# Optimization experiments

Measured on AMD Instinct MI355X. Metric: run time of the kernel, lower is better.

The kernel has to match this reference:

```python
import jax, jax.numpy as jnp
from jax import lax
import numpy as np

# dims (match init_kwargs config)
B, L, D = 32, 512, 32          # batch, seq_len, input_dim
H = 256                         # hidden_dim
E = 8                           # num_experts
PLEN, O = 96, 32                # pred_len, output_dim
LAT = 256                       # flow latent_dim
PD, NPROT = 64, 16              # prototype_dim, num_prototypes


def setup_inputs() -> dict:
    key = jax.random.key(0)
    ks = iter(jax.random.split(key, 40))
    def n(shape, scale=0.02):
        return (jax.random.normal(next(ks), shape, jnp.float32) * scale)
    inp = {
        'x': jax.random.normal(next(ks), (B, L, D), jnp.float32),
        # prototypes + projector (metric gating / diversity)
        'prototypes': n((NPROT, PD), 0.5),
        'Wp': n((PD, PD)), 'bp': jnp.zeros((PD,), jnp.float32),
        # expert_feature_extractor: Linear(7D->H), ReLU, Linear(H->PD), LayerNorm(PD)
        'Wf1': n((7 * D, H)), 'bf1': jnp.zeros((H,), jnp.float32),
        'Wf2': n((H, PD)), 'bf2': jnp.zeros((PD,), jnp.float32),
        'ln_g': jnp.ones((PD,), jnp.float32), 'ln_b': jnp.zeros((PD,), jnp.float32),
        # flow encoder (latent mapping of flattened window) + gating head
        'W1': n((L * D, H)), 'b1': jnp.zeros((H,), jnp.float32),
        'W2': n((H, LAT)), 'b2': jnp.zeros((LAT,), jnp.float32),
        'Wg': n((LAT, E)), 'bg': jnp.zeros((E,), jnp.float32),
        'log_temp': jnp.zeros((), jnp.float32),
        # stacked FFT+Mamba expert params (leading axis = expert)
        'Win': n((E, D, H)), 'b_in': jnp.zeros((E, H), jnp.float32),
        'Wfft': n((E, H, H)), 'b_fft': jnp.zeros((E, H), jnp.float32),
        'a_logit': n((E, H), 1.0),
        'Whead': n((E, H, PLEN * O)), 'b_head': jnp.zeros((E, PLEN * O), jnp.float32),
    }
    return inp


def _expert_features(x, Wf1, bf1, Wf2, bf2, ln_g, ln_b):
    # faithful to compute_expert_features: 7 per-channel stats -> MLP -> LayerNorm
    Lf = jnp.float32(x.shape[1])
    x_mean = x.mean(axis=1)
    x_std = x.std(axis=1, ddof=1)             # torch unbiased std
    x_min = x.min(axis=1)
    x_max = x.max(axis=1)
    x_diff_mean = jnp.diff(x, axis=1).mean(axis=1)
    x_trend = (x[:, -1, :] - x[:, 0, :]) / Lf
    x_fft_mag = jnp.abs(jnp.fft.fft(x, axis=1)).mean(axis=1)
    cf = jnp.concatenate([x_mean, x_std, x_min, x_max, x_diff_mean, x_trend, x_fft_mag], axis=1)
    h = jax.nn.relu(cf @ Wf1 + bf1)
    ef = h @ Wf2 + bf2
    mu = ef.mean(axis=-1, keepdims=True)
    var = ef.var(axis=-1, keepdims=True)
    return (ef - mu) / jnp.sqrt(var + 1e-5) * ln_g + ln_b


def reference(x, prototypes, Wp, bp, Wf1, bf1, Wf2, bf2, ln_g, ln_b,
              W1, b1, W2, b2, Wg, bg, log_temp,
              Win, b_in, Wfft, b_fft, a_logit, Whead, b_head):
    b, l, d = x.shape
    # --- metric-based gating ---
    ef = _expert_features(x, Wf1, bf1, Wf2, bf2, ln_g, ln_b)           # [B,PD]
    latent = jax.nn.relu(x.reshape(b, -1) @ W1 + b1) @ W2 + b2          # flow latent [B,LAT]
    lg = latent @ Wg + bg                                               # [B,E]
    proj = ef @ Wp + bp                                                 # prototype_projector
    d2 = ((proj[:, None, :] - prototypes[None, :, :]) ** 2).sum(-1)     # [B,NPROT]
    d2_per_expert = d2.reshape(b, E, NPROT // E).min(axis=-1)           # min dist to each expert's prototypes
    temp = jnp.clip(jnp.exp(log_temp), 0.1, 10.0)
    w = jax.nn.softmax((lg - d2_per_expert) / temp, axis=-1)            # [B,E]

    # --- FFT + Mamba-style experts (vmapped over stacked expert params) ---
    def expert(Win_e, b_in_e, Wfft_e, b_fft_e, a_logit_e, Whead_e, b_head_e):
        h = jnp.einsum('bld,dh->blh', x, Win_e) + b_in_e                # [B,L,H]
        f = jnp.einsum('blh,hk->blk', jnp.abs(jnp.fft.fft(h, axis=1)), Wfft_e) + b_fft_e
        u = jax.nn.relu(h + f)
        a = jax.nn.sigmoid(a_logit_e)                                   # per-channel decay
        def step(s, ut):
            s = a * s + (1.0 - a) * ut
            return s, None
        s_last, _ = lax.scan(step, jnp.zeros((b, H), x.dtype), jnp.swapaxes(u, 0, 1))
        return (s_last @ Whead_e + b_head_e).reshape(b, PLEN, O)

    outs = jax.vmap(expert)(Win, b_in, Wfft, b_fft, a_logit, Whead, b_head)  # [E,B,PLEN,O]
    y = jnp.einsum('be,ebpo->bpo', w, outs)
    return y
```

## Files before the change

### kernel.cpp

```cpp
#include <hip/hip_runtime.h>
#include <hip/hip_bf16.h>


typedef __hip_bfloat16 bf16;
typedef unsigned short u16;
typedef __attribute__((ext_vector_type(8))) short s8v;
typedef __attribute__((ext_vector_type(4))) float f4v;

#define MFMA_BF16(a,b,c) __builtin_amdgcn_mfma_f32_16x16x32_bf16(a,b,c,0,0,0)

#if __has_builtin(__builtin_amdgcn_sqrtf)
#define FSQRT(x) __builtin_amdgcn_sqrtf(x)
#else
#define FSQRT(x) sqrtf(x)
#endif
#if __has_builtin(__builtin_amdgcn_exp2f)
#define FEXP2(x) __builtin_amdgcn_exp2f(x)
#else
#define FEXP2(x) exp2f(x)
#endif
#if __has_builtin(__builtin_amdgcn_logf)
#define FLOG2(x) __builtin_amdgcn_logf(x)
#else
#define FLOG2(x) log2f(x)
#endif

#define GWF1 0
#define GW2  57344
#define GWF2 122880
#define GWP  139264
#define GPROT 143360
#define GWG  144384

__device__ __forceinline__ float bf2f(u16 u){
  union{ unsigned u32; float f; } w; w.u32 = ((unsigned)u) << 16; return w.f;
}
__device__ __forceinline__ u16 f2bf(float f){
  bf16 h = __float2bfloat16(f);
  union{ bf16 b; u16 u; } w; w.b = h; return w.u;
}
__device__ __forceinline__ u16 f2bf_fast(float f){
  union{ float f; unsigned u; } v; v.f = f;
  unsigned r = v.u + 0x7FFFu + ((v.u >> 16) & 1u);
  return (u16)(r >> 16);
}
__device__ __forceinline__ float ldg_(const void* p, long long i, bool bf){
  float r;
  if(bf) r = bf2f(((const u16*)p)[i]);
  else   r = ((const float*)p)[i];
  return r;
}
__device__ __forceinline__ bool bfflag(const void* ln_g){
  return ((const u16*)ln_g)[0] == 0x3F80;
}

__global__ __launch_bounds__(256) void ks1(const void* __restrict__ ln_g,
    const void* __restrict__ x,
    const void* __restrict__ Win, const void* __restrict__ Wfft,
    const void* __restrict__ W1, const void* __restrict__ Whead,
    const void* __restrict__ Wf1, const void* __restrict__ W2,
    const void* __restrict__ Wf2, const void* __restrict__ Wp,
    const void* __restrict__ prot, const void* __restrict__ Wg,
    u16* __restrict__ xbf,
    u16* __restrict__ WinTg, u16* __restrict__ WfftTg,
    u16* __restrict__ W1Tg, u16* __restrict__ WheadTg,
    u16* __restrict__ gw,
    u16* __restrict__ Xr, u16* __restrict__ Xi, float* __restrict__ cf){
  const bool bf = bfflag(ln_g);
  __shared__ float xs[512], re[512], im[512];
  __shared__ float twr[256], twi[256];
  __shared__ float r0s[4], r1s[4], r2s[4], r3s[4];
  __shared__ u16 tile[64][72];
  int BX = blockIdx.x, t = threadIdx.x;

  if(BX < 1024){
    int b = BX >> 5, d = BX & 31;
    {
      float rev = -(float)t * (1.f/512.f);
#if __has_builtin(__builtin_amdgcn_cosf) && __has_builtin(__builtin_amdgcn_sinf)
      twr[t] = __builtin_amdgcn_cosf(rev);
      twi[t] = __builtin_amdgcn_sinf(rev);
#else
      float ang = rev * 6.283185307179586f;
      twr[t] = cosf(ang); twi[t] = sinf(ang);
#endif
    }
    for(int i=t;i<512;i+=256){
      float v = ldg_(x, (long long)(b*512+i)*32 + d, bf);
      xs[i] = v;
      re[__brev((unsigned)i) >> 23] = v;
      im[i] = 0.f;
    }
    __syncthreads();
    float s=0.f, s2=0.f, mn=3.0e38f, mx=-3.0e38f;
    for(int i=t;i<512;i+=256){ float v=xs[i]; s+=v; s2+=v*v; mn=fminf(mn,v); mx=fmaxf(mx,v); }
    #pragma unroll
    for(int o=32;o>0;o>>=1){
      s  += __shfl_down(s,o);  s2 += __shfl_down(s2,o);
      mn = fminf(mn,__shfl_down(mn,o)); mx = fmaxf(mx,__shfl_down(mx,o));
    }
    int wv = t>>6, ln = t&63;
    if(ln==0){ r0s[wv]=s; r1s[wv]=s2; r2s[wv]=mn; r3s[wv]=mx; }
    __syncthreads();
    if(t==0){
      float S =r0s[0]+r0s[1]+r0s[2]+r0s[3];
      float S2=r1s[0]+r1s[1]+r1s[2]+r1s[3];
      float MN=fminf(fminf(r2s[0],r2s[1]),fminf(r2s[2],r2s[3]));
      float MX=fmaxf(fmaxf(r3s[0],r3s[1]),fmaxf(r3s[2],r3s[3]));
      float mean = S*(1.f/512.f);
      float var  = (S2 - S*S*(1.f/512.f))*(1.f/511.f);
      float* c = cf + b*224;
      c[d]      = mean;
      c[32+d]   = sqrtf(fmaxf(var,0.f));
      c[64+d]   = MN;
      c[96+d]   = MX;
      float dv = xs[511]-xs[0];
      c[128+d]  = dv*(1.f/511.f);
      c[160+d]  = dv*(1.f/512.f);
    }
    for(int st=1; st<=9; ++st){
      __syncthreads();
      int m = 1<<st, half = m>>1;
      int grp = t >> (st-1);
      int k   = t & (half-1);
      int i1 = grp*m + k, i2 = i1 + half;
      int ti_ = k << (9-st);
      float cs = twr[ti_], sn = twi[ti_];
      float ar=re[i1], ai=im[i1], br=re[i2], bi=im[i2];
      float tr = cs*br - sn*bi;
      float ti = cs*bi + sn*br;
      re[i1]=ar+tr; im[i1]=ai+ti;
      re[i2]=ar-tr; im[i2]=ai-ti;
    }
    __syncthreads();
    float ms=0.f;
    for(int i=t;i<512;i+=256){
      float rr=re[i], ii=im[i];
      long long o = (long long)(b*512+i)*32 + d;
      Xr[o]=f2bf(rr); Xi[o]=f2bf(ii);
      ms += FSQRT(rr*rr+ii*ii);
    }
    #pragma unroll
    for(int o=32;o>0;o>>=1) ms += __shfl_down(ms,o);
    if(ln==0) r0s[wv]=ms;
    __syncthreads();
    if(t==0) cf[b*224 + 192 + d] = (r0s[0]+r0s[1]+r0s[2]+r0s[3])*(1.f/512.f);
    return;
  }
  if(BX < 4111){
    int bx = BX - 1024;
    if(bx < 256){
      int i = bx*256 + t;
      int e = i >> 13, r = i & 8191;
      int c = r >> 5, d = r & 31;
      WinTg[i] = f2bf(ldg_(Win, (long long)e*8192 + d*256 + c, bf));
      return;
    }
    if(bx < 384){
      int idx = bx - 256;
      int e = idx >> 4, tl = idx & 15, kb = tl >> 2, cb = tl & 3;
      if(bf){
        for(int q=0;q<16;q++){
          int G = q*256 + t; int ki = G >> 6, ci = G & 63;
          tile[ci][ki] = ((const u16*)Wfft)[(long long)e*65536 + (long long)(kb*64+ki)*256 + cb*64+ci];
        }
      } else {
        for(int q=0;q<16;q++){
          int G = q*256 + t; int ki = G >> 6, ci = G & 63;
          tile[ci][ki] = f2bf(((const float*)Wfft)[(long long)e*65536 + (long long)(kb*64+ki)*256 + cb*64+ci]);
        }
      }
      __syncthreads();
      for(int q=0;q<16;q++){
        int G = q*256 + t; int ci = G >> 6, ki = G & 63;
        WfftTg[(long long)e*65536 + (long long)(cb*64+ci)*256 + kb*64+ki] = tile[ci][ki];
      }
      return;
    }
    if(bx < 1408){
      int idx = bx - 384;
      int kb = idx & 255, nb = idx >> 8;
      if(bf){
        for(int q=0;q<16;q++){
          int G = q*256 + t; int ki = G >> 6, ni = G & 63;
          tile[ni][ki] = ((const u16*)W1)[(long long)(kb*64+ki)*256 + nb*64+ni];
        }
      } else {
        for(int q=0;q<16;q++){
          int G = q*256 + t; int ki = G >> 6, ni = G & 63;
          tile[ni][ki] = f2bf(((const float*)W1)[(long long)(kb*64+ki)*256 + nb*64+ni]);
        }
      }
      __syncthreads();
      for(int q=0;q<16;q++){
        int G = q*256 + t; int ni = G >> 6, ki = G & 63;
        W1Tg[(long long)(nb*64+ni)*16384 + kb*64+ki] = tile[ni][ki];
      }
      return;
    }
    if(bx < 2944){
      int idx = bx - 1408;
      int e = idx / 192, rem = idx % 192;
      int kb = rem / 48, nb = rem % 48;
      if(bf){
        for(int q=0;q<16;q++){
          int G = q*256 + t; int ki = G >> 6, ni = G & 63;
          tile[ni][ki] = ((const u16*)Whead)[(long long)e*786432 + (long long)(kb*64+ki)*3072 + nb*64+ni];
        }
      } else {
        for(int q=0;q<16;q++){
          int G = q*256 + t; int ki = G >> 6, ni = G & 63;
          tile[ni][ki] = f2bf(((const float*)Whead)[(long long)e*786432 + (long long)(kb*64+ki)*3072 + nb*64+ni]);
        }
      }
      __syncthreads();
      for(int q=0;q<16;q++){
        int G = q*256 + t; int ni = G >> 6, ki = G & 63;
        WheadTg[(long long)e*786432 + (long long)(nb*64+ni)*256 + kb*64+ki] = tile[ni][ki];
      }
      return;
    }
    {
      int c = bx - 2944;
      const void* src; int dstbase, blkoff;
      if(c < 56)      { src=Wf1;  dstbase=GWF1;  blkoff=c; }
      else if(c <120) { src=W2;   dstbase=GW2;   blkoff=c-56; }
      else if(c <136) { src=Wf2;  dstbase=GWF2;  blkoff=c-120; }
      else if(c <140) { src=Wp;   dstbase=GWP;   blkoff=c-136; }
      else if(c <141) { src=prot; dstbase=GPROT; blkoff=0; }
      else            { src=Wg;   dstbase=GWG;   blkoff=c-141; }
      int i = blkoff*1024 + t*4;
      if(bf){
        ushort4 v = *(const ushort4*)((const u16*)src + i);
        *(ushort4*)(gw + dstbase + i) = v;
      } else {
        float4 f = *(const float4*)((const float*)src + i);
        ushort4 v; v.x=f2bf(f.x); v.y=f2bf(f.y); v.z=f2bf(f.z); v.w=f2bf(f.w);
        *(ushort4*)(gw + dstbase + i) = v;
      }
    }
    return;
  }
  {
    int i = ((BX-4111)*256 + t)*4;
    if(bf){
      ushort4 v = *(const ushort4*)((const u16*)x + i);
      *(ushort4*)(xbf+i) = v;
    } else {
      float4 f = *(const float4*)((const float*)x + i);
      ushort4 v; v.x=f2bf(f.x); v.y=f2bf(f.y); v.z=f2bf(f.z); v.w=f2bf(f.w);
      *(ushort4*)(xbf+i) = v;
    }
  }
}

__global__ __launch_bounds__(256) void ks2(const void* __restrict__ ln_g,
    const u16* __restrict__ xbf, const u16* __restrict__ Xr, const u16* __restrict__ Xi,
    const u16* __restrict__ WinTg, const u16* __restrict__ W1Tg,
    const void* __restrict__ b_in,
    float* __restrict__ psum, u16* __restrict__ hmagG){
  const bool bf = bfflag(ln_g);
  int BX = blockIdx.x, t = threadIdx.x;
  int w = t >> 6, lane = t & 63, quad = lane >> 4, l15 = lane & 15;
  const f4v zf = (f4v){0.f,0.f,0.f,0.f};
  __shared__ float binS[256];

  if(BX < 64){
    int kb = BX;
    f4v acc[2][4];
    #pragma unroll
    for(int mt=0;mt<2;mt++)
      #pragma unroll
      for(int nt=0;nt<4;nt++) acc[mt][nt] = zf;
    #pragma unroll
    for(int ks=0;ks<8;ks++){
      long long k = kb*256 + ks*32 + quad*8;
      s8v aF[2], bF[4];
      #pragma unroll
      for(int mt=0;mt<2;mt++)
        aF[mt] = *(const s8v*)(xbf + (long long)(mt*16 + l15)*16384 + k);
      #pragma unroll
      for(int nt=0;nt<4;nt++)
        bF[nt] = *(const s8v*)(W1Tg + (long long)(w*64 + nt*16 + l15)*16384 + k);
      #pragma unroll
      for(int mt=0;mt<2;mt++)
        #pragma unroll
        for(int nt=0;nt<4;nt++)
          acc[mt][nt] = MFMA_BF16(aF[mt], bF[nt], acc[mt][nt]);
    }
    float* po = psum + (long long)kb*8192;
    #pragma unroll
    for(int mt=0;mt<2;mt++)
      #pragma unroll
      for(int nt=0;nt<4;nt++)
        #pragma unroll
        for(int r=0;r<4;r++)
          po[(mt*16 + quad*4 + r)*256 + w*64 + nt*16 + l15] = acc[mt][nt][r];
    return;
  }
  {
    int bx = BX - 64;
    int e = bx >> 7, inner = bx & 127;
    int b = inner >> 2, half = (inner >> 1) & 1, kh = inner & 1;
    int row0 = b*512 + half*128;
    binS[t] = ldg_(b_in, e*256+t, bf);
    s8v xrF[2], xiF[2];
    #pragma unroll
    for(int nt=0;nt<2;nt++){
      long long row = row0 + w*32 + nt*16 + l15;
      xrF[nt] = *(const s8v*)(Xr + row*32 + quad*8);
      xiF[nt] = *(const s8v*)(Xi + row*32 + quad*8);
    }
    __syncthreads();
    u16* Ho = hmagG + (long long)((e<<6)|(b<<1)|half)*32768;
    #pragma unroll
    for(int kcl=0;kcl<2;kcl++){
      int k0 = (kh*2+kcl)*64;
      #pragma unroll
      for(int ct=0;ct<4;ct++){
        s8v wfr = *(const s8v*)(WinTg + ((long long)e*256 + k0 + ct*16 + l15)*32 + quad*8);
        #pragma unroll
        for(int nt=0;nt<2;nt++){
          f4v hr = MFMA_BF16(wfr, xrF[nt], zf);
          f4v hi = MFMA_BF16(wfr, xiF[nt], zf);
          int rowg = row0 + w*32 + nt*16 + l15;
          bool bin0 = ((rowg & 511) == 0);
          ushort4 pk;
          int cb4 = k0 + ct*16 + quad*4;
          float h0 = hr[0] + (bin0 ? 512.f*binS[cb4+0] : 0.f);
          float h1 = hr[1] + (bin0 ? 512.f*binS[cb4+1] : 0.f);
          float h2 = hr[2] + (bin0 ? 512.f*binS[cb4+2] : 0.f);
          float h3 = hr[3] + (bin0 ? 512.f*binS[cb4+3] : 0.f);
          pk.x = f2bf_fast(FSQRT(h0*h0 + hi[0]*hi[0]));
          pk.y = f2bf_fast(FSQRT(h1*h1 + hi[1]*hi[1]));
          pk.z = f2bf_fast(FSQRT(h2*h2 + hi[2]*hi[2]));
          pk.w = f2bf_fast(FSQRT(h3*h3 + hi[3]*hi[3]));
          *(ushort4*)&Ho[(w*32 + nt*16 + l15)*256 + cb4] = pk;
        }
      }
    }
  }
}

__global__ __launch_bounds__(256) void ks3(const void* __restrict__ ln_g,
    const float* __restrict__ cf, const float* __restrict__ psum,
    const u16* __restrict__ gw,
    const void* __restrict__ bf1, const void* __restrict__ b1,
    const u16* __restrict__ xbf, const u16* __restrict__ hmagG,
    const u16* __restrict__ WinTg, const u16* __restrict__ WfftTg,
    const void* __restrict__ b_in, const void* __restrict__ b_fft,
    const void* __restrict__ a_logit,
    float* __restrict__ hsf, float* __restrict__ h1f, float* __restrict__ sp){
  const bool bf = bfflag(ln_g);
  int BX = blockIdx.x, t = threadIdx.x;
  __shared__ __align__(16) u16 BsT[128][72];
  __shared__ float biasS[128], l2aS[128], aS[128];
  __shared__ float cfs[224];

  if(BX < 64){
    int bx = BX;
    if(bx < 32){
      int b = bx;
      float s0=0.f, s1=0.f, s2=0.f, s3=0.f;
      #pragma unroll
      for(int kb=0;kb<64;kb+=4){
        s0 += psum[(long long)(kb+0)*8192 + b*256 + t];
        s1 += psum[(long long)(kb+1)*8192 + b*256 + t];
        s2 += psum[(long long)(kb+2)*8192 + b*256 + t];
        s3 += psum[(long long)(kb+3)*8192 + b*256 + t];
      }
      hsf[b*256+t] = fmaxf((s0+s1)+(s2+s3) + ldg_(b1,t,bf), 0.f);
    } else {
      int b = bx - 32;
      if(t < 224) cfs[t] = cf[(long long)b*224 + t];
      __syncthreads();
      float a1 = ldg_(bf1, t, bf);
      const u16* Wp_ = gw + GWF1 + t;
      #pragma unroll 16
      for(int k=0;k<224;k++) a1 += cfs[k]*bf2f(Wp_[k*256]);
      h1f[b*256+t] = fmaxf(a1, 0.f);
    }
    return;
  }
  {
    int bx = BX - 64;
    int e = bx >> 7, inner = bx & 127;
    int b = inner >> 2, half = (inner >> 1) & 1, cb = inner & 1;
    int row0 = b*512 + half*128;
    int col0 = cb*128;
    int w = t >> 6, lane = t & 63, quad = lane >> 4, l15 = lane & 15;

    if(t < 128){
      int c = col0 + t;
      biasS[t] = ldg_(b_in, e*256+c, bf) + ldg_(b_fft, e*256+c, bf);
      float a = 1.f/(1.f+__expf(-ldg_(a_logit, e*256+c, bf)));
      a = fminf(fmaxf(a, 1e-12f), 0.99999988f);
      aS[t] = a;
      l2aS[t] = FLOG2(a);
    }
    const u16* Ab = hmagG + (long long)((e<<6)|(b<<1)|half)*32768;
    const f4v zf = (f4v){0.f,0.f,0.f,0.f};
    f4v acc[2][8];
    #pragma unroll
    for(int mt=0;mt<2;mt++)
      #pragma unroll
      for(int nt=0;nt<8;nt++) acc[mt][nt] = zf;

    for(int kc=0;kc<4;kc++){
      int k0 = kc*64;
      __syncthreads();
      #pragma unroll
      for(int q=0;q<4;q++){
        int G = q*256 + t;
        int c = G >> 3, k8 = (G & 7)*8;
        *(s8v*)&BsT[c][k8] = *(const s8v*)(WfftTg + ((long long)e*256 + col0 + c)*256 + k0 + k8);
      }
      __syncthreads();
      #pragma unroll
      for(int ks=0;ks<2;ks++){
        int kb = ks*32 + quad*8;
        s8v aF0 = *(const s8v*)(Ab + (w*32 + l15)*256 + k0 + kb);
        s8v aF1 = *(const s8v*)(Ab + (w*32 + 16 + l15)*256 + k0 + kb);
        #pragma unroll
        for(int nt=0;nt<8;nt++){
          s8v bF = *(const s8v*)&BsT[nt*16 + l15][kb];
          acc[0][nt] = MFMA_BF16(aF0, bF, acc[0][nt]);
          acc[1][nt] = MFMA_BF16(aF1, bF, acc[1][nt]);
        }
      }
    }
    s8v xF[2], xFm[2];
    #pragma unroll
    for(int mt=0;mt<2;mt++){
      long long rowO = (long long)row0 + w*32 + mt*16 + l15;
      xF[mt] = *(const s8v*)(xbf + rowO*32 + quad*8);
      int lin = half*128 + w*32 + mt*16 + l15;
      int lm  = (512 - lin) & 511;
      xFm[mt] = *(const s8v*)(xbf + ((long long)b*512 + lm)*32 + quad*8);
    }
    int l0base = half*128 + w*32 + quad*4;
    float mz = (l0base == 0) ? 0.f : 1.f;
    const f4v zf2 = (f4v){0.f,0.f,0.f,0.f};
    float part[8];
    #pragma unroll
    for(int nt=0;nt<8;nt++){
      s8v wfh = *(const s8v*)(WinTg + ((long long)e*256 + col0 + nt*16 + l15)*32 + quad*8);
      f4v hv0 = MFMA_BF16(xF[0],  wfh, zf2);
      f4v hv1 = MFMA_BF16(xF[1],  wfh, zf2);
      f4v hm0 = MFMA_BF16(xFm[0], wfh, zf2);
      f4v hm1 = MFMA_BF16(xFm[1], wfh, zf2);
      int cl = nt*16 + l15;
      float l2a = l2aS[cl], bias = biasS[cl], av = aS[cl];
      float inv_a = FEXP2(-l2a);
      float cO0 = FEXP2(l2a * (float)(511 - l0base));
      float cO1 = FEXP2(l2a * (float)(495 - l0base));
      float cM0 = FEXP2(l2a * (float)(l0base - 1));
      float cM1 = FEXP2(l2a * (float)(l0base + 15));
      float sum = 0.f;
      #pragma unroll
      for(int r=0;r<4;r++){
        float u0 = fmaxf(acc[0][nt][r] + hv0[r] + bias, 0.f);
        sum += u0 * cO0;
        float u1 = fmaxf(acc[1][nt][r] + hv1[r] + bias, 0.f);
        sum += u1 * cO1;
        float m0 = fmaxf(acc[0][nt][r] + hm0[r] + bias, 0.f);
        float w0 = m0 * cM0;
        if(r == 0) w0 *= mz;
        sum += w0;
        float m1 = fmaxf(acc[1][nt][r] + hm1[r] + bias, 0.f);
        sum += m1 * cM1;
        cO0 *= inv_a; cO1 *= inv_a; cM0 *= av; cM1 *= av;
      }
      part[nt] = sum;
    }
    __syncthreads();
    float (*redS)[132] = (float(*)[132])BsT;
    #pragma unroll
    for(int nt=0;nt<8;nt++)
      redS[w*4 + quad][nt*16 + l15] = part[nt];
    __syncthreads();
    if(t < 128){
      float tot = 0.f;
      #pragma unroll
      for(int i=0;i<16;i++) tot += redS[i][t];
      sp[e*16384 + (b*2 + half)*256 + col0 + t] = tot;
    }
  }
}

__global__ __launch_bounds__(256) void ks4(const void* __restrict__ ln_g,
    const float* __restrict__ hsf, const float* __restrict__ h1f,
    const u16* __restrict__ gw,
    const void* __restrict__ bf2, const void* __restrict__ ln_b,
    const void* __restrict__ bp, const void* __restrict__ b2,
    const void* __restrict__ bg, const void* __restrict__ log_temp,
    const float* __restrict__ sp, const void* __restrict__ a_logit,
    const void* __restrict__ b_in, const void* __restrict__ b_fft,
    const u16* __restrict__ xbf, const u16* __restrict__ Xr,
    const u16* __restrict__ Xi,
    const void* __restrict__ Win, const void* __restrict__ Wfft,
    float* __restrict__ wgt, u16* __restrict__ ssbf){
  const bool bf = bfflag(ln_g);
  int BX = blockIdx.x, t = threadIdx.x;
  __shared__ float hsL[256], h1L[256], latL[256], efL[64], prL[64];
  __shared__ float red[4][64];
  __shared__ float d2part[16][16], d2s[16], lgpart[32][8];
  __shared__ float hm[256];
  __shared__ float xr6[32], xi6[32], x6[32];

  if(BX < 32){
    int b = BX;
    hsL[t] = hsf[b*256+t];
    h1L[t] = h1f[b*256+t];
    __syncthreads();
    {
      float a = ldg_(b2, t, bf);
      const u16* W2p = gw + GW2 + t;
      #pragma unroll 16
      for(int k=0;k<256;k++) a += hsL[k]*bf2f(W2p[k*256]);
      latL[t] = a;
    }
    {
      int p = t>>6, j = t&63;
      float acc = 0.f;
      const u16* Wf2p = gw + GWF2 + p*64*64 + j;
      #pragma unroll 16
      for(int i=0;i<64;i++) acc += h1L[p*64+i]*bf2f(Wf2p[i*64]);
      red[p][j] = acc;
    }
    __syncthreads();
    if(t < 64){
      float a2 = red[0][t]+red[1][t]+red[2][t]+red[3][t] + ldg_(bf2,t,bf);
      float sm=a2, sq=a2*a2;
      #pragma unroll
      for(int o=32;o>0;o>>=1){ sm += __shfl_xor(sm,o); sq += __shfl_xor(sq,o); }
      float mu  = sm*(1.f/64.f);
      float var = sq*(1.f/64.f) - mu*mu;
      efL[t] = (a2-mu)*rsqrtf(fmaxf(var,0.f)+1e-5f)*ldg_(ln_g,t,bf) + ldg_(ln_b,t,bf);
      float p_acc = ldg_(bp, t, bf);
      const u16* Wpp = gw + GWP + t;
      #pragma unroll 16
      for(int k=0;k<64;k++) p_acc += efL[k]*bf2f(Wpp[k*64]);
      prL[t] = p_acc;
    }
    {
      int part = t>>3, e = t&7;
      float gp = 0.f;
      const u16* Wgp = gw + GWG + e;
      #pragma unroll
      for(int i=0;i<8;i++){
        int k = part*8 + i;
        gp += latL[k]*bf2f(Wgp[k*8]);
      }
      lgpart[part][e] = gp;
    }
    __syncthreads();
    {
      int p = t>>4, q4 = t&15;
      float dd = 0.f;
      #pragma unroll
      for(int i=0;i<4;i++){
        int d = q4*4 + i;
        float df = prL[d] - bf2f(gw[GPROT + p*64 + d]);
        dd += df*df;
      }
      d2part[p][q4] = dd;
    }
    __syncthreads();
    if(t < 16){
      float s = 0.f;
      #pragma unroll
      for(int i=0;i<16;i++) s += d2part[t][i];
      d2s[t] = s;
    }
    __syncthreads();
    if(t < 8){
      float g = ldg_(bg, t, bf);
      #pragma unroll
      for(int p=0;p<32;p++) g += lgpart[p][t];
      float d2pe = fminf(d2s[2*t], d2s[2*t+1]);
      float temp = fminf(fmaxf(__expf(ldg_(log_temp,0,bf)), 0.1f), 10.f);
      float v = (g - d2pe) / temp;
      float m = v;
      m = fmaxf(m, __shfl_xor(m,1));
      m = fmaxf(m, __shfl_xor(m,2));
      m = fmaxf(m, __shfl_xor(m,4));
      float ex = __expf(v-m);
      float sum = ex;
      sum += __shfl_xor(sum,1);
      sum += __shfl_xor(sum,2);
      sum += __shfl_xor(sum,4);
      wgt[b*8+t] = ex/sum;
    }
    return;
  }
  {
    int bx = BX - 32;
    int e = bx >> 5, b = bx & 31, j = t;
    if(j < 32){
      long long o = ((long long)(b*512 + 256))*32 + j;
      xr6[j] = bf2f(Xr[o]);
      xi6[j] = bf2f(Xi[o]);
      x6[j]  = bf2f(xbf[o]);
    }
    __syncthreads();
    float sr=0.f, si=0.f, hx=0.f;
    if(bf){
      const u16* Wn = (const u16*)Win + (long long)e*8192 + j;
      #pragma unroll 8
      for(int d=0; d<32; d++){
        float wv = bf2f(Wn[d*256]);
        sr += xr6[d]*wv; si += xi6[d]*wv; hx += x6[d]*wv;
      }
    } else {
      const float* Wn = (const float*)Win + (long long)e*8192 + j;
      #pragma unroll 8
      for(int d=0; d<32; d++){
        float wv = Wn[d*256];
        sr += xr6[d]*wv; si += xi6[d]*wv; hx += x6[d]*wv;
      }
    }
    hm[j] = FSQRT(sr*sr + si*si);
    __syncthreads();
    float f = 0.f;
    if(bf){
      const u16* Wf = (const u16*)Wfft + (long long)e*65536 + j;
      #pragma unroll 8
      for(int k=0;k<256;k++) f += hm[k]*bf2f(Wf[(long long)k*256]);
    } else {
      const float* Wf = (const float*)Wfft + (long long)e*65536 + j;
      #pragma unroll 8
      for(int k=0;k<256;k++) f += hm[k]*Wf[(long long)k*256];
    }
    float a = 1.f/(1.f+__expf(-ldg_(a_logit, e*256+j, bf)));
    a = fminf(fmaxf(a, 1e-12f), 0.99999988f);
    float l2a = FLOG2(a);
    float u = fmaxf(hx + f + ldg_(b_in,e*256+j,bf) + ldg_(b_fft,e*256+j,bf), 0.f);
    float contrib = u * FEXP2(l2a * 255.f);
    const float* spe = sp + e*16384 + b*2*256;
    float sum = spe[j] + spe[256+j] + contrib;
    ssbf[(e*32+b)*256 + j] = f2bf((1.f-a)*sum);
  }
}

__global__ __launch_bounds__(256) void k6_mfma(
    const u16* __restrict__ ssbf, const u16* __restrict__ WheadTg,
    float* __restrict__ yaccE){
  int nb = blockIdx.x, e = blockIdx.y;
  int t = threadIdx.x;
  int w = t >> 6, lane = t & 63, quad = lane >> 4, l15 = lane & 15;
  const f4v zf = (f4v){0.f,0.f,0.f,0.f};
  f4v acc[2][2];
  #pragma unroll
  for(int mt=0;mt<2;mt++)
    #pragma unroll
    for(int nt=0;nt<2;nt++) acc[mt][nt] = zf;
  #pragma unroll
  for(int ks=0;ks<8;ks++){
    int k = ks*32 + quad*8;
    s8v aF[2], bF[2];
    #pragma unroll
    for(int mt=0;mt<2;mt++)
      aF[mt] = *(const s8v*)(ssbf + (long long)(e*32 + mt*16 + l15)*256 + k);
    #pragma unroll
    for(int nt=0;nt<2;nt++)
      bF[nt] = *(const s8v*)(WheadTg + ((long long)e*3072 + nb*128 + w*32 + nt*16 + l15)*256 + k);
    #pragma unroll
    for(int mt=0;mt<2;mt++)
      #pragma unroll
      for(int nt=0;nt<2;nt++)
        acc[mt][nt] = MFMA_BF16(aF[mt], bF[nt], acc[mt][nt]);
  }
  float* yo = yaccE + (long long)e*98304;
  #pragma unroll
  for(int mt=0;mt<2;mt++)
    #pragma unroll
    for(int nt=0;nt<2;nt++){
      int col = nb*128 + w*32 + nt*16 + l15;
      #pragma unroll
      for(int r=0;r<4;r++){
        int b = mt*16 + quad*4 + r;
        yo[b*3072 + col] = acc[mt][nt][r];
      }
    }
}

__global__ void k7_out(const void* __restrict__ ln_g,
                       const float* __restrict__ yaccE,
                       const float* __restrict__ wgt,
                       const void* __restrict__ b_head,
                       void* __restrict__ out){
  const bool bf = bfflag(ln_g);
  int i = blockIdx.x*256 + threadIdx.x;
  int b = i / 3072, col = i - b*3072;
  float v = 0.f;
  #pragma unroll
  for(int e=0;e<8;e++)
    v += wgt[b*8+e]*(yaccE[(long long)e*98304 + i] + ldg_(b_head, (long long)e*3072+col, bf));
  if(bf) ((u16*)out)[i] = f2bf(v);
  else   ((float*)out)[i] = v;
}

extern "C" void kernel_launch(void* const* d_in, const int* in_sizes, int n_in,
                              void* d_out, int out_size, void* d_ws, size_t ws_size,
                              hipStream_t stream){
  const void* x       = d_in[0];
  const void* prot    = d_in[1];
  const void* Wp      = d_in[2];
  const void* bp      = d_in[3];
  const void* Wf1     = d_in[4];
  const void* bf1     = d_in[5];
  const void* Wf2     = d_in[6];
  const void* bf2     = d_in[7];
  const void* ln_g    = d_in[8];
  const void* ln_b    = d_in[9];
  const void* W1      = d_in[10];
  const void* b1      = d_in[11];
  const void* W2      = d_in[12];
  const void* b2      = d_in[13];
  const void* Wg      = d_in[14];
  const void* bg      = d_in[15];
  const void* log_temp= d_in[16];
  const void* Win     = d_in[17];
  const void* b_in    = d_in[18];
  const void* Wfft    = d_in[19];
  const void* b_fft   = d_in[20];
  const void* a_logit = d_in[21];
  const void* Whead   = d_in[22];
  const void* b_head  = d_in[23];

  float* ws      = (float*)d_ws;
  float* cf      = ws;
  float* wgt     = cf + 7168;
  float* sp      = wgt + 256;
  float* hsf     = sp + 131072;
  float* h1f     = hsf + 8192;
  float* yaccE   = sp + 262144;
  float* psum    = yaccE + 786432;
  u16*   Xr      = (u16*)(psum + 524288);
  u16*   Xi      = Xr + 524288;
  u16*   xbf     = Xi + 524288;
  u16*   WinTg   = xbf + 524288;
  u16*   WfftTg  = WinTg + 65536;
  u16*   W1Tg    = WfftTg + 524288;
  u16*   WheadTg = W1Tg + 4194304;
  u16*   ssbf    = WheadTg + 6291456;
  u16*   gw      = ssbf + 65536;
  u16*   hmagG   = gw + 146432;

  ks1 <<<dim3(4623), dim3(256), 0, stream>>>(ln_g, x, Win, Wfft, W1, Whead,
                                             Wf1, W2, Wf2, Wp, prot, Wg,
                                             xbf, WinTg, WfftTg, W1Tg, WheadTg, gw,
                                             Xr, Xi, cf);
  ks2 <<<dim3(1088), dim3(256), 0, stream>>>(ln_g, xbf, Xr, Xi, WinTg, W1Tg,
                                             b_in, psum, hmagG);
  ks3 <<<dim3(1088), dim3(256), 0, stream>>>(ln_g, cf, psum, gw, bf1, b1,
                                             xbf, hmagG, WinTg, WfftTg,
                                             b_in, b_fft, a_logit,
                                             hsf, h1f, sp);
  ks4 <<<dim3(288),  dim3(256), 0, stream>>>(ln_g, hsf, h1f, gw, bf2, ln_b,
                                             bp, b2, bg, log_temp,
                                             sp, a_logit, b_in, b_fft,
                                             xbf, Xr, Xi, Win, Wfft,
                                             wgt, ssbf);
  k6_mfma <<<dim3(24,8), dim3(256), 0, stream>>>(ssbf, WheadTg, yaccE);
  k7_out  <<<dim3(384),  dim3(256), 0, stream>>>(ln_g, yaccE, wgt, b_head, d_out);
}
```

Before: 204.9 us.

## Fold gating and expert tail into earlier kernels; fuse head GEMM with mixture

Moves the h1 feature MLP and the per-expert last-step contribution into ks2, and the gating softmax into ks3. The head GEMM and the weighted expert mixture become one kernel, k67, which loops over experts, builds the scaled state in shared memory and writes the output directly. This drops two launches and the yaccE, hsf and ssbf intermediates. In exchange, the fused head kernel runs only 24 blocks that walk all 8 experts in sequence, so far fewer CUs share the Whead streaming.

```diff
diff --git a/kernel.cpp b/kernel.cpp
--- a/kernel.cpp
+++ b/kernel.cpp
@@ -257,13 +257,20 @@
 __global__ __launch_bounds__(256) void ks2(const void* __restrict__ ln_g,
     const u16* __restrict__ xbf, const u16* __restrict__ Xr, const u16* __restrict__ Xi,
     const u16* __restrict__ WinTg, const u16* __restrict__ W1Tg,
-    const void* __restrict__ b_in,
-    float* __restrict__ psum, u16* __restrict__ hmagG){
+    const u16* __restrict__ gw, const float* __restrict__ cf,
+    const void* __restrict__ bf1, const void* __restrict__ b_in,
+    const void* __restrict__ b_fft, const void* __restrict__ a_logit,
+    const void* __restrict__ Win, const void* __restrict__ Wfft,
+    float* __restrict__ psum, u16* __restrict__ hmagG,
+    float* __restrict__ h1f, float* __restrict__ contrib){
   const bool bf = bfflag(ln_g);
   int BX = blockIdx.x, t = threadIdx.x;
   int w = t >> 6, lane = t & 63, quad = lane >> 4, l15 = lane & 15;
   const f4v zf = (f4v){0.f,0.f,0.f,0.f};
   __shared__ float binS[256];
+  __shared__ float cfs[224];
+  __shared__ float hm[256];
+  __shared__ float xr6[32], xi6[32], x6[32];
 
   if(BX < 64){
     int kb = BX;
@@ -298,7 +305,7 @@
           po[(mt*16 + quad*4 + r)*256 + w*64 + nt*16 + l15] = acc[mt][nt][r];
     return;
   }
-  {
+  if(BX < 1088){
     int bx = BX - 64;
     int e = bx >> 7, inner = bx & 127;
     int b = inner >> 2, half = (inner >> 1) & 1, kh = inner & 1;
@@ -339,28 +346,88 @@
         }
       }
     }
+    return;
+  }
+  if(BX < 1120){
+    int b = BX - 1088;
+    if(t < 224) cfs[t] = cf[(long long)b*224 + t];
+    __syncthreads();
+    float a1 = ldg_(bf1, t, bf);
+    const u16* Wp_ = gw + GWF1 + t;
+    #pragma unroll 16
+    for(int k=0;k<224;k++) a1 += cfs[k]*bf2f(Wp_[k*256]);
+    h1f[b*256+t] = fmaxf(a1, 0.f);
+    return;
+  }
+  {
+    int bx = BX - 1120;
+    int e = bx >> 5, b = bx & 31, j = t;
+    if(j < 32){
+      long long o = ((long long)(b*512 + 256))*32 + j;
+      xr6[j] = bf2f(Xr[o]);
+      xi6[j] = bf2f(Xi[o]);
+      x6[j]  = bf2f(xbf[o]);
+    }
+    __syncthreads();
+    float sr=0.f, si=0.f, hx=0.f;
+    if(bf){
+      const u16* Wn = (const u16*)Win + (long long)e*8192 + j;
+      #pragma unroll 8
+      for(int d=0; d<32; d++){
+        float wv = bf2f(Wn[d*256]);
+        sr += xr6[d]*wv; si += xi6[d]*wv; hx += x6[d]*wv;
+      }
+    } else {
+      const float* Wn = (const float*)Win + (long long)e*8192 + j;
+      #pragma unroll 8
+      for(int d=0; d<32; d++){
+        float wv = Wn[d*256];
+        sr += xr6[d]*wv; si += xi6[d]*wv; hx += x6[d]*wv;
+      }
+    }
+    hm[j] = FSQRT(sr*sr + si*si);
+    __syncthreads();
+    float f = 0.f;
+    if(bf){
+      const u16* Wf = (const u16*)Wfft + (long long)e*65536 + j;
+      #pragma unroll 8
+      for(int k=0;k<256;k++) f += hm[k]*bf2f(Wf[(long long)k*256]);
+    } else {
+      const float* Wf = (const float*)Wfft + (long long)e*65536 + j;
+      #pragma unroll 8
+      for(int k=0;k<256;k++) f += hm[k]*Wf[(long long)k*256];
+    }
+    float a = 1.f/(1.f+__expf(-ldg_(a_logit, e*256+j, bf)));
+    a = fminf(fmaxf(a, 1e-12f), 0.99999988f);
+    float l2a = FLOG2(a);
+    float u = fmaxf(hx + f + ldg_(b_in,e*256+j,bf) + ldg_(b_fft,e*256+j,bf), 0.f);
+    contrib[(e*32+b)*256 + j] = u * FEXP2(l2a * 255.f);
   }
 }
 
 __global__ __launch_bounds__(256) void ks3(const void* __restrict__ ln_g,
-    const float* __restrict__ cf, const float* __restrict__ psum,
+    const float* __restrict__ psum, const float* __restrict__ h1f,
     const u16* __restrict__ gw,
-    const void* __restrict__ bf1, const void* __restrict__ b1,
+    const void* __restrict__ b1, const void* __restrict__ bf2,
+    const void* __restrict__ ln_b, const void* __restrict__ bp,
+    const void* __restrict__ b2, const void* __restrict__ bg,
+    const void* __restrict__ log_temp,
     const u16* __restrict__ xbf, const u16* __restrict__ hmagG,
     const u16* __restrict__ WinTg, const u16* __restrict__ WfftTg,
     const void* __restrict__ b_in, const void* __restrict__ b_fft,
     const void* __restrict__ a_logit,
-    float* __restrict__ hsf, float* __restrict__ h1f, float* __restrict__ sp){
+    float* __restrict__ wgt, float* __restrict__ sp){
   const bool bf = bfflag(ln_g);
   int BX = blockIdx.x, t = threadIdx.x;
   __shared__ __align__(16) u16 BsT[128][72];
   __shared__ float biasS[128], l2aS[128], aS[128];
-  __shared__ float cfs[224];
-
-  if(BX < 64){
-    int bx = BX;
-    if(bx < 32){
-      int b = bx;
+  __shared__ float hsL[256], h1L[256], latL[256], efL[64], prL[64];
+  __shared__ float red[4][64];
+  __shared__ float d2part[16][16], d2s[16], lgpart[32][8];
+
+  if(BX < 32){
+    int b = BX;
+    {
       float s0=0.f, s1=0.f, s2=0.f, s3=0.f;
       #pragma unroll
       for(int kb=0;kb<64;kb+=4){
@@ -369,21 +436,93 @@
         s2 += psum[(long long)(kb+2)*8192 + b*256 + t];
         s3 += psum[(long long)(kb+3)*8192 + b*256 + t];
       }
-      hsf[b*256+t] = fmaxf((s0+s1)+(s2+s3) + ldg_(b1,t,bf), 0.f);
-    } else {
-      int b = bx - 32;
-      if(t < 224) cfs[t] = cf[(long long)b*224 + t];
-      __syncthreads();
-      float a1 = ldg_(bf1, t, bf);
-      const u16* Wp_ = gw + GWF1 + t;
+      hsL[t] = fmaxf((s0+s1)+(s2+s3) + ldg_(b1,t,bf), 0.f);
+    }
+    h1L[t] = h1f[b*256+t];
+    __syncthreads();
+    {
+      float a = ldg_(b2, t, bf);
+      const u16* W2p = gw + GW2 + t;
       #pragma unroll 16
-      for(int k=0;k<224;k++) a1 += cfs[k]*bf2f(Wp_[k*256]);
-      h1f[b*256+t] = fmaxf(a1, 0.f);
+      for(int k=0;k<256;k++) a += hsL[k]*bf2f(W2p[k*256]);
+      latL[t] = a;
+    }
+    {
+      int p = t>>6, j = t&63;
+      float acc = 0.f;
+      const u16* Wf2p = gw + GWF2 + p*64*64 + j;
+      #pragma unroll 16
+      for(int i=0;i<64;i++) acc += h1L[p*64+i]*bf2f(Wf2p[i*64]);
+      red[p][j] = acc;
+    }
+    __syncthreads();
+    if(t < 64){
+      float a2 = red[0][t]+red[1][t]+red[2][t]+red[3][t] + ldg_(bf2,t,bf);
+      float sm=a2, sq=a2*a2;
+      #pragma unroll
+      for(int o=32;o>0;o>>=1){ sm += __shfl_xor(sm,o); sq += __shfl_xor(sq,o); }
+      float mu  = sm*(1.f/64.f);
+      float var = sq*(1.f/64.f) - mu*mu;
+      efL[t] = (a2-mu)*rsqrtf(fmaxf(var,0.f)+1e-5f)*ldg_(ln_g,t,bf) + ldg_(ln_b,t,bf);
+      float p_acc = ldg_(bp, t, bf);
+      const u16* Wpp = gw + GWP + t;
+      #pragma unroll 16
+      for(int k=0;k<64;k++) p_acc += efL[k]*bf2f(Wpp[k*64]);
+      prL[t] = p_acc;
+    }
+    {
+      int part = t>>3, e = t&7;
+      float gp = 0.f;
+      const u16* Wgp = gw + GWG + e;
+      #pragma unroll
+      for(int i=0;i<8;i++){
+        int k = part*8 + i;
+        gp += latL[k]*bf2f(Wgp[k*8]);
+      }
+      lgpart[part][e] = gp;
+    }
+    __syncthreads();
+    {
+      int p = t>>4, q4 = t&15;
+      float dd = 0.f;
+      #pragma unroll
+      for(int i=0;i<4;i++){
+        int d = q4*4 + i;
+        float df = prL[d] - bf2f(gw[GPROT + p*64 + d]);
+        dd += df*df;
+      }
+      d2part[p][q4] = dd;
+    }
+    __syncthreads();
+    if(t < 16){
+      float s = 0.f;
+      #pragma unroll
+      for(int i=0;i<16;i++) s += d2part[t][i];
+      d2s[t] = s;
+    }
+    __syncthreads();
+    if(t < 8){
+      float g = ldg_(bg, t, bf);
+      #pragma unroll
+      for(int p=0;p<32;p++) g += lgpart[p][t];
+      float d2pe = fminf(d2s[2*t], d2s[2*t+1]);
+      float temp = fminf(fmaxf(__expf(ldg_(log_temp,0,bf)), 0.1f), 10.f);
+      float v = (g - d2pe) / temp;
+      float m = v;
+      m = fmaxf(m, __shfl_xor(m,1));
+      m = fmaxf(m, __shfl_xor(m,2));
+      m = fmaxf(m, __shfl_xor(m,4));
+      float ex = __expf(v-m);
+      float sum = ex;
+      sum += __shfl_xor(sum,1);
+      sum += __shfl_xor(sum,2);
+      sum += __shfl_xor(sum,4);
+      wgt[b*8+t] = ex/sum;
     }
     return;
   }
   {
-    int bx = BX - 64;
+    int bx = BX - 32;
     int e = bx >> 7, inner = bx & 127;
     int b = inner >> 2, half = (inner >> 1) & 1, cb = inner & 1;
     int row0 = b*512 + half*128;
@@ -488,190 +627,78 @@
   }
 }
 
-__global__ __launch_bounds__(256) void ks4(const void* __restrict__ ln_g,
-    const float* __restrict__ hsf, const float* __restrict__ h1f,
-    const u16* __restrict__ gw,
-    const void* __restrict__ bf2, const void* __restrict__ ln_b,
-    const void* __restrict__ bp, const void* __restrict__ b2,
-    const void* __restrict__ bg, const void* __restrict__ log_temp,
-    const float* __restrict__ sp, const void* __restrict__ a_logit,
-    const void* __restrict__ b_in, const void* __restrict__ b_fft,
-    const u16* __restrict__ xbf, const u16* __restrict__ Xr,
-    const u16* __restrict__ Xi,
-    const void* __restrict__ Win, const void* __restrict__ Wfft,
-    float* __restrict__ wgt, u16* __restrict__ ssbf){
+__global__ __launch_bounds__(256) void k67(const void* __restrict__ ln_g,
+    const float* __restrict__ sp, const float* __restrict__ contrib,
+    const float* __restrict__ wgt, const void* __restrict__ a_logit,
+    const u16* __restrict__ WheadTg, const void* __restrict__ b_head,
+    void* __restrict__ out){
   const bool bf = bfflag(ln_g);
-  int BX = blockIdx.x, t = threadIdx.x;
-  __shared__ float hsL[256], h1L[256], latL[256], efL[64], prL[64];
-  __shared__ float red[4][64];
-  __shared__ float d2part[16][16], d2s[16], lgpart[32][8];
-  __shared__ float hm[256];
-  __shared__ float xr6[32], xi6[32], x6[32];
-
-  if(BX < 32){
-    int b = BX;
-    hsL[t] = hsf[b*256+t];
-    h1L[t] = h1f[b*256+t];
-    __syncthreads();
-    {
-      float a = ldg_(b2, t, bf);
-      const u16* W2p = gw + GW2 + t;
-      #pragma unroll 16
-      for(int k=0;k<256;k++) a += hsL[k]*bf2f(W2p[k*256]);
-      latL[t] = a;
-    }
-    {
-      int p = t>>6, j = t&63;
-      float acc = 0.f;
-      const u16* Wf2p = gw + GWF2 + p*64*64 + j;
-      #pragma unroll 16
-      for(int i=0;i<64;i++) acc += h1L[p*64+i]*bf2f(Wf2p[i*64]);
-      red[p][j] = acc;
-    }
-    __syncthreads();
-    if(t < 64){
-      float a2 = red[0][t]+red[1][t]+red[2][t]+red[3][t] + ldg_(bf2,t,bf);
-      float sm=a2, sq=a2*a2;
-      #pragma unroll
-      for(int o=32;o>0;o>>=1){ sm += __shfl_xor(sm,o); sq += __shfl_xor(sq,o); }
-      float mu  = sm*(1.f/64.f);
-      float var = sq*(1.f/64.f) - mu*mu;
-      efL[t] = (a2-mu)*rsqrtf(fmaxf(var,0.f)+1e-5f)*ldg_(ln_g,t,bf) + ldg_(ln_b,t,bf);
-      float p_acc = ldg_(bp, t, bf);
-      const u16* Wpp = gw + GWP + t;
-      #pragma unroll 16
-      for(int k=0;k<64;k++) p_acc += efL[k]*bf2f(Wpp[k*64]);
-      prL[t] = p_acc;
-    }
-    {
-      int part = t>>3, e = t&7;
-      float gp = 0.f;
-      const u16* Wgp = gw + GWG + e;
-      #pragma unroll
-      for(int i=0;i<8;i++){
-        int k = part*8 + i;
-        gp += latL[k]*bf2f(Wgp[k*8]);
-      }
-      lgpart[part][e] = gp;
-    }
-    __syncthreads();
-    {
-      int p = t>>4, q4 = t&15;
-      float dd = 0.f;
-      #pragma unroll
-      for(int i=0;i<4;i++){
-        int d = q4*4 + i;
-        float df = prL[d] - bf2f(gw[GPROT + p*64 + d]);
-        dd += df*df;
-      }
-      d2part[p][q4] = dd;
-    }
-    __syncthreads();
-    if(t < 16){
-      float s = 0.f;
-      #pragma unroll
-      for(int i=0;i<16;i++) s += d2part[t][i];
-      d2s[t] = s;
-    }
-    __syncthreads();
-    if(t < 8){
-      float g = ldg_(bg, t, bf);
-      #pragma unroll
-      for(int p=0;p<32;p++) g += lgpart[p][t];
-      float d2pe = fminf(d2s[2*t], d2s[2*t+1]);
-      float temp = fminf(fmaxf(__expf(ldg_(log_temp,0,bf)), 0.1f), 10.f);
-      float v = (g - d2pe) / temp;
-      float m = v;
-      m = fmaxf(m, __shfl_xor(m,1));
-      m = fmaxf(m, __shfl_xor(m,2));
-      m = fmaxf(m, __shfl_xor(m,4));
-      float ex = __expf(v-m);
-      float sum = ex;
-      sum += __shfl_xor(sum,1);
-      sum += __shfl_xor(sum,2);
-      sum += __shfl_xor(sum,4);
-      wgt[b*8+t] = ex/sum;
-    }
-    return;
-  }
-  {
-    int bx = BX - 32;
-    int e = bx >> 5, b = bx & 31, j = t;
-    if(j < 32){
-      long long o = ((long long)(b*512 + 256))*32 + j;
-      xr6[j] = bf2f(Xr[o]);
-      xi6[j] = bf2f(Xi[o]);
-      x6[j]  = bf2f(xbf[o]);
-    }
-    __syncthreads();
-    float sr=0.f, si=0.f, hx=0.f;
-    if(bf){
-      const u16* Wn = (const u16*)Win + (long long)e*8192 + j;
-      #pragma unroll 8
-      for(int d=0; d<32; d++){
-        float wv = bf2f(Wn[d*256]);
-        sr += xr6[d]*wv; si += xi6[d]*wv; hx += x6[d]*wv;
-      }
-    } else {
-      const float* Wn = (const float*)Win + (long long)e*8192 + j;
-      #pragma unroll 8
-      for(int d=0; d<32; d++){
-        float wv = Wn[d*256];
-        sr += xr6[d]*wv; si += xi6[d]*wv; hx += x6[d]*wv;
-      }
-    }
-    hm[j] = FSQRT(sr*sr + si*si);
-    __syncthreads();
-    float f = 0.f;
-    if(bf){
-      const u16* Wf = (const u16*)Wfft + (long long)e*65536 + j;
-      #pragma unroll 8
-      for(int k=0;k<256;k++) f += hm[k]*bf2f(Wf[(long long)k*256]);
-    } else {
-      const float* Wf = (const float*)Wfft + (long long)e*65536 + j;
-      #pragma unroll 8
-      for(int k=0;k<256;k++) f += hm[k]*Wf[(long long)k*256];
-    }
-    float a = 1.f/(1.f+__expf(-ldg_(a_logit, e*256+j, bf)));
+  int nb = blockIdx.x, t = threadIdx.x;
+  int w = t >> 6, lane = t & 63, quad = lane >> 4, l15 = lane & 15;
+  __shared__ __align__(16) u16 ssS[32][264];
+  __shared__ float omaS[2048];
+  __shared__ float wgtS[256];
+
+  wgtS[t] = wgt[t];
+  #pragma unroll
+  for(int q=0;q<8;q++){
+    int idx = q*256 + t;
+    float a = 1.f/(1.f+__expf(-ldg_(a_logit, idx, bf)));
     a = fminf(fmaxf(a, 1e-12f), 0.99999988f);
-    float l2a = FLOG2(a);
-    float u = fmaxf(hx + f + ldg_(b_in,e*256+j,bf) + ldg_(b_fft,e*256+j,bf), 0.f);
-    float contrib = u * FEXP2(l2a * 255.f);
-    const float* spe = sp + e*16384 + b*2*256;
-    float sum = spe[j] + spe[256+j] + contrib;
-    ssbf[(e*32+b)*256 + j] = f2bf((1.f-a)*sum);
-  }
-}
-
-__global__ __launch_bounds__(256) void k6_mfma(
-    const u16* __restrict__ ssbf, const u16* __restrict__ WheadTg,
-    float* __restrict__ yaccE){
-  int nb = blockIdx.x, e = blockIdx.y;
-  int t = threadIdx.x;
-  int w = t >> 6, lane = t & 63, quad = lane >> 4, l15 = lane & 15;
+    omaS[idx] = 1.f - a;
+  }
   const f4v zf = (f4v){0.f,0.f,0.f,0.f};
   f4v acc[2][2];
   #pragma unroll
   for(int mt=0;mt<2;mt++)
     #pragma unroll
     for(int nt=0;nt<2;nt++) acc[mt][nt] = zf;
-  #pragma unroll
-  for(int ks=0;ks<8;ks++){
-    int k = ks*32 + quad*8;
-    s8v aF[2], bF[2];
+
+  for(int e=0;e<8;e++){
+    __syncthreads();
+    {
+      float oma = omaS[e*256 + t];
+      const float* sp0 = sp + e*16384 + t;
+      const float* cb  = contrib + e*8192 + t;
+      #pragma unroll
+      for(int q=0;q<32;q++){
+        float v = oma*(sp0[q*512] + sp0[q*512+256] + cb[q*256]);
+        ssS[q][t] = f2bf(v);
+      }
+    }
+    __syncthreads();
+    f4v tmp[2][2];
     #pragma unroll
     for(int mt=0;mt<2;mt++)
-      aF[mt] = *(const s8v*)(ssbf + (long long)(e*32 + mt*16 + l15)*256 + k);
-    #pragma unroll
-    for(int nt=0;nt<2;nt++)
-      bF[nt] = *(const s8v*)(WheadTg + ((long long)e*3072 + nb*128 + w*32 + nt*16 + l15)*256 + k);
-    #pragma unroll
-    for(int mt=0;mt<2;mt++)
+      #pragma unroll
+      for(int nt=0;nt<2;nt++) tmp[mt][nt] = zf;
+    #pragma unroll
+    for(int ks=0;ks<8;ks++){
+      int k = ks*32 + quad*8;
+      s8v aF0 = *(const s8v*)&ssS[l15][k];
+      s8v aF1 = *(const s8v*)&ssS[16 + l15][k];
+      s8v bF[2];
       #pragma unroll
       for(int nt=0;nt<2;nt++)
-        acc[mt][nt] = MFMA_BF16(aF[mt], bF[nt], acc[mt][nt]);
-  }
-  float* yo = yaccE + (long long)e*98304;
+        bF[nt] = *(const s8v*)(WheadTg + ((long long)e*3072 + nb*128 + w*32 + nt*16 + l15)*256 + k);
+      tmp[0][0] = MFMA_BF16(aF0, bF[0], tmp[0][0]);
+      tmp[0][1] = MFMA_BF16(aF0, bF[1], tmp[0][1]);
+      tmp[1][0] = MFMA_BF16(aF1, bF[0], tmp[1][0]);
+      tmp[1][1] = MFMA_BF16(aF1, bF[1], tmp[1][1]);
+    }
+    #pragma unroll
+    for(int nt=0;nt<2;nt++){
+      int col = nb*128 + w*32 + nt*16 + l15;
+      float bh = ldg_(b_head, (long long)e*3072 + col, bf);
+      #pragma unroll
+      for(int mt=0;mt<2;mt++)
+        #pragma unroll
+        for(int r=0;r<4;r++){
+          int b = mt*16 + quad*4 + r;
+          acc[mt][nt][r] += wgtS[b*8+e]*(tmp[mt][nt][r] + bh);
+        }
+    }
+  }
   #pragma unroll
   for(int mt=0;mt<2;mt++)
     #pragma unroll
@@ -680,25 +707,11 @@
       #pragma unroll
       for(int r=0;r<4;r++){
         int b = mt*16 + quad*4 + r;
-        yo[b*3072 + col] = acc[mt][nt][r];
-      }
-    }
-}
-
-__global__ void k7_out(const void* __restrict__ ln_g,
-                       const float* __restrict__ yaccE,
-                       const float* __restrict__ wgt,
-                       const void* __restrict__ b_head,
-                       void* __restrict__ out){
-  const bool bf = bfflag(ln_g);
-  int i = blockIdx.x*256 + threadIdx.x;
-  int b = i / 3072, col = i - b*3072;
-  float v = 0.f;
-  #pragma unroll
-  for(int e=0;e<8;e++)
-    v += wgt[b*8+e]*(yaccE[(long long)e*98304 + i] + ldg_(b_head, (long long)e*3072+col, bf));
-  if(bf) ((u16*)out)[i] = f2bf(v);
-  else   ((float*)out)[i] = v;
+        long long i = (long long)b*3072 + col;
+        if(bf) ((u16*)out)[i] = f2bf(acc[mt][nt][r]);
+        else   ((float*)out)[i] = acc[mt][nt][r];
+      }
+    }
 }
 
 extern "C" void kernel_launch(void* const* d_in, const int* in_sizes, int n_in,
@@ -733,10 +746,9 @@
   float* cf      = ws;
   float* wgt     = cf + 7168;
   float* sp      = wgt + 256;
-  float* hsf     = sp + 131072;
-  float* h1f     = hsf + 8192;
-  float* yaccE   = sp + 262144;
-  float* psum    = yaccE + 786432;
+  float* h1f     = sp + 131072;
+  float* contrib = sp + 262144;
+  float* psum    = sp + 262144 + 786432;
   u16*   Xr      = (u16*)(psum + 524288);
   u16*   Xi      = Xr + 524288;
   u16*   xbf     = Xi + 524288;
@@ -752,17 +764,15 @@
                                              Wf1, W2, Wf2, Wp, prot, Wg,
                                              xbf, WinTg, WfftTg, W1Tg, WheadTg, gw,
                                              Xr, Xi, cf);
-  ks2 <<<dim3(1088), dim3(256), 0, stream>>>(ln_g, xbf, Xr, Xi, WinTg, W1Tg,
-                                             b_in, psum, hmagG);
-  ks3 <<<dim3(1088), dim3(256), 0, stream>>>(ln_g, cf, psum, gw, bf1, b1,
+  ks2 <<<dim3(1376), dim3(256), 0, stream>>>(ln_g, xbf, Xr, Xi, WinTg, W1Tg,
+                                             gw, cf, bf1, b_in, b_fft, a_logit,
+                                             Win, Wfft,
+                                             psum, hmagG, h1f, contrib);
+  ks3 <<<dim3(1056), dim3(256), 0, stream>>>(ln_g, psum, h1f, gw,
+                                             b1, bf2, ln_b, bp, b2, bg, log_temp,
                                              xbf, hmagG, WinTg, WfftTg,
                                              b_in, b_fft, a_logit,
-                                             hsf, h1f, sp);
-  ks4 <<<dim3(288),  dim3(256), 0, stream>>>(ln_g, hsf, h1f, gw, bf2, ln_b,
-                                             bp, b2, bg, log_temp,
-                                             sp, a_logit, b_in, b_fft,
-                                             xbf, Xr, Xi, Win, Wfft,
-                                             wgt, ssbf);
-  k6_mfma <<<dim3(24,8), dim3(256), 0, stream>>>(ssbf, WheadTg, yaccE);
-  k7_out  <<<dim3(384),  dim3(256), 0, stream>>>(ln_g, yaccE, wgt, b_head, d_out);
-}
+                                             wgt, sp);
+  k67 <<<dim3(24),   dim3(256), 0, stream>>>(ln_g, sp, contrib, wgt, a_logit,
+                                             WheadTg, b_head, d_out);
+}
```

Result: slower. 224.6 us (+9.6%).
